# Optimization experiments

Measured on AMD Instinct MI355X. Metric: run time of the kernel, lower is better.

## Reference

```python
import jax, jax.numpy as jnp
import numpy as np

WS = 8   # window_size
SS = 4   # shift_size
NH = 8   # num_heads


def _shift_mask(ws, ss):
    """Faithful port of _create_shift_mask (returns [1,1,ws,ws])."""
    m = np.zeros((ws, ws), np.float32)
    cnt = 0
    for hs in (slice(0, ws - ss), slice(ws - ss, ws)):
        for wsl in (slice(0, ws - ss), slice(ws - ss, ws)):
            m[hs, wsl] = cnt
            cnt += 1
    shifted = np.roll(m, (-ss, -ss), (0, 1))
    return (m != shifted).astype(np.float32)[None, None]

_MASK = jnp.asarray(_shift_mask(WS, SS))  # all-ones when ss == ws/2 (as in source)


def window_partition(x, ws):
    # [B,C,H,W] -> [B*nWin, C, ws, ws]
    B, C, H, W = x.shape
    x = x.reshape(B, C, H // ws, ws, W // ws, ws)
    x = x.transpose(0, 2, 4, 1, 3, 5)
    return x.reshape(-1, C, ws, ws)


def window_merge(x, H, W, ws):
    # [B*nWin, C, ws, ws] -> [B,C,H,W]
    C = x.shape[1]
    B = x.shape[0] // ((H // ws) * (W // ws))
    x = x.reshape(B, H // ws, W // ws, C, ws, ws)
    x = x.transpose(0, 3, 1, 4, 2, 5)
    return x.reshape(B, C, H, W)


def conv1x1(x, w):
    # 1x1 conv, no bias: weight [Cout, Cin]
    return jnp.einsum('oc,bchw->bohw', w, x)


def win_attention(q, k, v, temperature):
    # q,k,v: [Bw, C, ws, ws]; temperature: [nh,1,1]
    Bw, C, wh, ww = q.shape
    hd = C // NH
    N = wh * ww
    def heads(t):
        return t.reshape(Bw, NH, hd, N).transpose(0, 1, 3, 2)  # [Bw,nh,N,hd]
    q, k, v = heads(q), heads(k), heads(v)
    attn = jnp.einsum('bhnd,bhmd->bhnm', q, k) * temperature  # temp broadcasts per-head
    attn = jax.nn.softmax(attn, axis=-1)
    out = jnp.einsum('bhnm,bhmd->bhnd', attn, v)
    return out.transpose(0, 1, 3, 2).reshape(Bw, C, wh, ww)


def _branch(x_q, x_kv, temperature, Wq, Wk, Wv, Wo):
    xq_w = window_partition(x_q, WS)
    xkv_w = window_partition(x_kv, WS)
    q = conv1x1(xq_w, Wq)
    k = conv1x1(xkv_w, Wk)
    v = conv1x1(xkv_w, Wv)
    a = win_attention(q, k, v, temperature)
    return conv1x1(a, Wo)  # [B*nWin, C, ws, ws]


def setup_inputs() -> dict:
    key = jax.random.key(0)
    ks = jax.random.split(key, 6)
    B, C, H, W = 2, 256, 192, 192
    return {
        'x_q': jax.random.normal(ks[0], (B, C, H, W), jnp.float32),
        'x_kv': jax.random.normal(ks[1], (B, C, H, W), jnp.float32),
        'temperature': jnp.ones((NH, 1, 1), jnp.float32),
        'Wq': jax.random.normal(ks[2], (C, C), jnp.float32) * 0.02,
        'Wk': jax.random.normal(ks[3], (C, C), jnp.float32) * 0.02,
        'Wv': jax.random.normal(ks[4], (C, C), jnp.float32) * 0.02,
        'Wo': jax.random.normal(ks[5], (C, C), jnp.float32) * 0.02,
    }


def reference(x_q, x_kv, temperature, Wq, Wk, Wv, Wo):
    B, C, H, W = x_q.shape
    # unshifted branch
    out_win = _branch(x_q, x_kv, temperature, Wq, Wk, Wv, Wo)
    out = window_merge(out_win, H, W, WS)
    # shifted branch
    xq_s = jnp.roll(x_q, shift=(-SS, -SS), axis=(2, 3))
    xkv_s = jnp.roll(x_kv, shift=(-SS, -SS), axis=(2, 3))
    out_s = _branch(xq_s, xkv_s, temperature, Wq, Wk, Wv, Wo)
    out_s = out_s * (1.0 - _MASK)  # zero overlap regions (all-ones mask here)
    out_s = window_merge(out_s, H, W, WS)
    out_s = jnp.roll(out_s, shift=(SS, SS), axis=(2, 3))
    return out + out_s
```

## Files before the change

### kernel.cpp

```cpp
#include <hip/hip_runtime.h>
#include <hip/hip_bf16.h>


typedef short bf16x4 __attribute__((ext_vector_type(4)));
typedef short bf16x8 __attribute__((ext_vector_type(8)));
typedef float f32x4  __attribute__((ext_vector_type(4)));
typedef unsigned short ushort_t;

#define MFMA_K16(A_, B_, C_) __builtin_amdgcn_mfma_f32_16x16x16bf16_1k((A_), (B_), (C_), 0, 0, 0)
#define MFMA_K32(A_, B_, C_) __builtin_amdgcn_mfma_f32_16x16x32_bf16((A_), (B_), (C_), 0, 0, 0)

__device__ __forceinline__ short f2b(float f) {
  __hip_bfloat16 h = __float2bfloat16(f);
  return __builtin_bit_cast(short, h);
}
__device__ __forceinline__ bf16x4 cvt4(f32x4 v, float sc) {
  bf16x4 r;
  r[0] = f2b(v[0] * sc); r[1] = f2b(v[1] * sc);
  r[2] = f2b(v[2] * sc); r[3] = f2b(v[3] * sc);
  return r;
}
__device__ __forceinline__ int PI(int p) { return (p ^ (p >> 3)) & 7; }

template<bool B16>
__device__ __forceinline__ bf16x8 ldw8(const void* W, int row, int c0) {
  if constexpr (B16) {
    return *(const bf16x8*)((const ushort_t*)W + (row << 8) + c0);
  } else {
    const float* p = (const float*)W + (row << 8) + c0;
    const float4 x = *(const float4*)p, y = *(const float4*)(p + 4);
    bf16x8 f;
    f[0] = f2b(x.x); f[1] = f2b(x.y); f[2] = f2b(x.z); f[3] = f2b(x.w);
    f[4] = f2b(y.x); f[5] = f2b(y.y); f[6] = f2b(y.z); f[7] = f2b(y.w);
    return f;
  }
}
__device__ __forceinline__ bf16x8 ldw8b(const ushort_t* W, int row, int c0) {
  return *(const bf16x8*)(W + (row << 8) + c0);
}

constexpr size_t BUFE = 9437184;

__global__ void wconv(const float* __restrict__ a, const float* __restrict__ b,
                      const float* __restrict__ c, const float* __restrict__ d,
                      ushort_t* __restrict__ o) {
  const int gid = blockIdx.x * 256 + threadIdx.x;
  const int which = gid >> 14;
  const int idx = (gid & 16383) * 4;
  const float* src = which == 0 ? a : which == 1 ? b : which == 2 ? c : d;
  const float4 v = *(const float4*)(src + idx);
  bf16x4 w; w[0] = f2b(v.x); w[1] = f2b(v.y); w[2] = f2b(v.z); w[3] = f2b(v.w);
  *(bf16x4*)(o + which * 65536 + idx) = w;
}

__global__ __launch_bounds__(256, 4) void g0_xt(
    const float* __restrict__ xq, const float* __restrict__ xkv,
    ushort_t* __restrict__ xtq, ushort_t* __restrict__ xtkv, int bbase)
{
  __shared__ __align__(16) ushort_t tile[64 * 72];
  const int tid = threadIdx.x;
  const int id = (blockIdx.x & 7) * (gridDim.x >> 3) + (blockIdx.x >> 3);
  int r = id;
  const int pxt = r % 576; r /= 576;
  const int ct = r & 3; r >>= 2;
  const int which = r & 1;
  const int bl = r >> 1;
  const float* src = which ? xkv : xq;
  ushort_t* dst = which ? xtkv : xtq;
  const size_t gib = (size_t)(bbase + bl) * BUFE;

  {
    const int cr = tid >> 2, seg = tid & 3;
    const float* p = src + gib + (size_t)(ct * 64 + cr) * 36864 + pxt * 64 + seg * 16;
    const float4 f0 = *(const float4*)p,       f1 = *(const float4*)(p + 4);
    const float4 f2 = *(const float4*)(p + 8), f3 = *(const float4*)(p + 12);
    bf16x8 a, b;
    a[0]=f2b(f0.x); a[1]=f2b(f0.y); a[2]=f2b(f0.z); a[3]=f2b(f0.w);
    a[4]=f2b(f1.x); a[5]=f2b(f1.y); a[6]=f2b(f1.z); a[7]=f2b(f1.w);
    b[0]=f2b(f2.x); b[1]=f2b(f2.y); b[2]=f2b(f2.z); b[3]=f2b(f2.w);
    b[4]=f2b(f3.x); b[5]=f2b(f3.y); b[6]=f2b(f3.z); b[7]=f2b(f3.w);
    *(bf16x8*)(tile + cr * 72 + seg * 16) = a;
    *(bf16x8*)(tile + cr * 72 + seg * 16 + 8) = b;
  }
  __syncthreads();
  {
    const int opx = tid >> 2, oseg = tid & 3;
    bf16x8 a, b;
    #pragma unroll
    for (int j = 0; j < 8; ++j) a[j] = tile[(oseg * 16 + j) * 72 + opx];
    #pragma unroll
    for (int j = 0; j < 8; ++j) b[j] = tile[(oseg * 16 + 8 + j) * 72 + opx];
    ushort_t* q = dst + (size_t)bl * BUFE + (size_t)(pxt * 64 + opx) * 256 + ct * 64 + oseg * 16;
    *(bf16x8*)q = a;
    *(bf16x8*)(q + 8) = b;
  }
}

__global__ __launch_bounds__(256, 4) void g1_qkv(
    const ushort_t* __restrict__ xtq, const ushort_t* __restrict__ xtkv,
    const ushort_t* __restrict__ Wq, const ushort_t* __restrict__ Wk,
    const ushort_t* __restrict__ Wv,
    ushort_t* __restrict__ qbuf, ushort_t* __restrict__ kbuf,
    ushort_t* __restrict__ vimg)
{
  __shared__ __align__(16) char smem[24576];
  const int tid = threadIdx.x, lane = tid & 63, wv4 = tid >> 6;
  const int l15 = lane & 15, g = lane >> 4;

  const int wid = (blockIdx.x & 7) * (gridDim.x >> 3) + (blockIdx.x >> 3);
  const int ct = wid % 6;
  int r = wid / 6;
  const int whalf = r & 1; r >>= 1;
  const int h = r % 192;
  const int bl = r / 192;
  const int wstart = whalf * 96, ph = h & 7;
  const int winbase = bl * 576 + (h >> 3) * 24 + whalf * 12;
  const int pxrow = h * 192 + wstart;

  const int mode = ct >> 1;
  const ushort_t* xs = ((mode == 0) ? xtq : xtkv) + (size_t)bl * BUFE;
  const ushort_t* W  = (mode == 0) ? Wq : (mode == 1) ? Wk : Wv;
  const int cobase = (ct & 1) * 128 + wv4 * 32;

  f32x4 acc[6][2];
  #pragma unroll
  for (int nt = 0; nt < 6; ++nt) { acc[nt][0] = {0,0,0,0}; acc[nt][1] = {0,0,0,0}; }

  #pragma unroll
  for (int ki = 0; ki < 2; ++ki) {
    if (ki) __syncthreads();
    #pragma unroll
    for (int j = 0; j < 6; ++j) {
      const int u = j * 256 + tid;
      const int t = u >> 4, ch = u & 15;
      const bf16x8 v = *(const bf16x8*)(xs + (size_t)(pxrow + t) * 256 + ki * 128 + ch * 8);
      const int sl = ch ^ (t & 7);
      *(bf16x8*)(smem + (unsigned)(t * 256 + sl * 16)) = v;
    }
    __syncthreads();
    #pragma unroll
    for (int sk = 0; sk < 4; ++sk) {
      const int c0 = ki * 128 + sk * 32 + g * 8;
      const bf16x8 w0 = ldw8b(W, cobase + l15,      c0);
      const bf16x8 w1 = ldw8b(W, cobase + 16 + l15, c0);
      #pragma unroll
      for (int nt = 0; nt < 6; ++nt) {
        const int t = nt * 16 + l15;
        const int lch = sk * 4 + g;
        const bf16x8 af = *(const bf16x8*)(smem + (unsigned)(t * 256 + ((lch ^ (t & 7)) << 4)));
        if (mode < 2) {
          acc[nt][0] = MFMA_K32(w0, af, acc[nt][0]);
          acc[nt][1] = MFMA_K32(w1, af, acc[nt][1]);
        } else {
          acc[nt][0] = MFMA_K32(af, w0, acc[nt][0]);
          acc[nt][1] = MFMA_K32(af, w1, acc[nt][1]);
        }
      }
    }
  }

  if (mode < 2) {
    ushort_t* dst = (mode == 0) ? qbuf : kbuf;
    #pragma unroll
    for (int nt = 0; nt < 6; ++nt)
      #pragma unroll
      for (int cj = 0; cj < 2; ++cj) {
        const int t = nt * 16 + l15;
        const int win = winbase + (t >> 3);
        const int pos = ph * 8 + (t & 7);
        const int co = cobase + cj * 16 + 4 * g;
        *(bf16x4*)(dst + (size_t)win * 16384 + pos * 256 + co) = cvt4(acc[nt][cj], 1.f);
      }
  } else {
    #pragma unroll
    for (int nt = 0; nt < 6; ++nt)
      #pragma unroll
      for (int dj = 0; dj < 2; ++dj) {
        const int t0 = nt * 16 + 4 * g;
        const int d = cobase + dj * 16 + l15;
        *(bf16x4*)(vimg + (size_t)bl * BUFE + (size_t)d * 36864 + pxrow + t0)
            = cvt4(acc[nt][dj], 1.f);
      }
  }
}

__global__ __launch_bounds__(256, 4) void attn2(
    const float* __restrict__ temp,
    const ushort_t* __restrict__ qbuf, const ushort_t* __restrict__ kbuf,
    const ushort_t* __restrict__ vimg, ushort_t* __restrict__ abuf)
{
  const int tid = threadIdx.x, lane = tid & 63, wv4 = tid >> 6;
  const int l15 = lane & 15, g = lane >> 4;

  const int wid = (blockIdx.x & 7) * (gridDim.x >> 3) + (blockIdx.x >> 3);
  const int hg = wid & 1;
  const int winL = wid >> 1;
  const int bl = winL / 576, rw = winL % 576;
  const int wh = rw / 24, ww = rw % 24;
  const int h = hg * 4 + wv4;
  const float tm = temp[h];
  const size_t wb = (size_t)winL * 16384;
  const int hb = h * 32;
  const f32x4 fzero = {0.f, 0.f, 0.f, 0.f};

  bf16x8 qf[4], kf[4];
  #pragma unroll
  for (int i = 0; i < 4; ++i) {
    qf[i] = *(const bf16x8*)(qbuf + wb + (i * 16 + l15) * 256 + hb + g * 8);
    kf[i] = *(const bf16x8*)(kbuf + wb + (i * 16 + l15) * 256 + hb + g * 8);
  }
  f32x4 s[4][4];
  #pragma unroll
  for (int mt = 0; mt < 4; ++mt)
    #pragma unroll
    for (int nt = 0; nt < 4; ++nt)
      s[mt][nt] = MFMA_K32(kf[mt], qf[nt], fzero);

  bf16x4 Pb[4][4];
  #pragma unroll
  for (int nt = 0; nt < 4; ++nt) {
    float mx = -1e30f;
    #pragma unroll
    for (int mt = 0; mt < 4; ++mt)
      #pragma unroll
      for (int rr = 0; rr < 4; ++rr) {
        const float v = s[mt][nt][rr] * tm;
        s[mt][nt][rr] = v;
        mx = fmaxf(mx, v);
      }
    mx = fmaxf(mx, __shfl_xor(mx, 16));
    mx = fmaxf(mx, __shfl_xor(mx, 32));
    float sum = 0.f;
    #pragma unroll
    for (int mt = 0; mt < 4; ++mt)
      #pragma unroll
      for (int rr = 0; rr < 4; ++rr) {
        const float p = __expf(s[mt][nt][rr] - mx);
        s[mt][nt][rr] = p;
        sum += p;
      }
    sum += __shfl_xor(sum, 16);
    sum += __shfl_xor(sum, 32);
    const float ri = 1.f / sum;
    #pragma unroll
    for (int mt = 0; mt < 4; ++mt) Pb[mt][nt] = cvt4(s[mt][nt], ri);
  }

  f32x4 pcd[2][4];
  #pragma unroll
  for (int dj = 0; dj < 2; ++dj)
    #pragma unroll
    for (int nt = 0; nt < 4; ++nt) pcd[dj][nt] = fzero;
  #pragma unroll
  for (int mt = 0; mt < 4; ++mt)
    #pragma unroll
    for (int dj = 0; dj < 2; ++dj) {
      const int d = hb + dj * 16 + l15;
      const bf16x4 vf = *(const bf16x4*)(vimg + (size_t)bl * BUFE + (size_t)d * 36864
                        + (wh * 8 + 2 * mt + (g >> 1)) * 192 + ww * 8 + 4 * (g & 1));
      #pragma unroll
      for (int nt = 0; nt < 4; ++nt)
        pcd[dj][nt] = MFMA_K16(vf, Pb[mt][nt], pcd[dj][nt]);
    }

  #pragma unroll
  for (int dj = 0; dj < 2; ++dj)
    #pragma unroll
    for (int nt = 0; nt < 4; ++nt) {
      const int pos = nt * 16 + l15;
      const int c0 = hb + dj * 16 + 4 * g;
      *(bf16x4*)(abuf + wb + pos * 256 + c0) = cvt4(pcd[dj][nt], 1.f);
    }
}

__global__ __launch_bounds__(256, 4) void k2_out(
    const ushort_t* __restrict__ Wo, const ushort_t* __restrict__ abuf,
    float* __restrict__ out, int bbase)
{
  __shared__ __align__(16) char smem[24576];
  const int tid = threadIdx.x, lane = tid & 63, wv4 = tid >> 6;
  const int l15 = lane & 15, g = lane >> 4;

  const int wid = (blockIdx.x & 7) * (gridDim.x >> 3) + (blockIdx.x >> 3);
  const int ct = wid & 1;
  int r = wid >> 1;
  const int whalf = r & 1; r >>= 1;
  const int h = r % 192, bl = r / 192;
  const int wh = h >> 3, ph = h & 7, wstart = whalf * 96;
  const int winbase = bl * 576 + wh * 24 + (wstart >> 3);

  f32x4 acc[6][2];
  #pragma unroll
  for (int nt = 0; nt < 6; ++nt) { acc[nt][0] = {0,0,0,0}; acc[nt][1] = {0,0,0,0}; }

  const int corow0 = ct * 128 + wv4 * 32 + l15;

  #pragma unroll
  for (int ki = 0; ki < 2; ++ki) {
    const int kb = ki * 128;
    if (ki) __syncthreads();
    #pragma unroll
    for (int j = 0; j < 6; ++j) {
      const int u = j * 256 + tid;
      const int t = u >> 4, ch = u & 15;
      const int win = winbase + (t >> 3);
      const int wpos = ph * 8 + (t & 7);
      const bf16x8 v = *(const bf16x8*)(abuf + (size_t)win * 16384 + wpos * 256 + kb + ch * 8);
      const int sl = ch ^ (t & 7);
      *(bf16x8*)(smem + (unsigned)(t * 256 + sl * 16)) = v;
    }
    __syncthreads();
    #pragma unroll
    for (int sk = 0; sk < 4; ++sk) {
      const int c0 = kb + sk * 32 + g * 8;
      const bf16x8 w0 = ldw8b(Wo, corow0,      c0);
      const bf16x8 w1 = ldw8b(Wo, corow0 + 16, c0);
      #pragma unroll
      for (int nt = 0; nt < 6; ++nt) {
        const int t = nt * 16 + l15;
        const int lch = sk * 4 + g;
        const bf16x8 af = *(const bf16x8*)(smem + (unsigned)(t * 256 + ((lch ^ (t & 7)) << 4)));
        acc[nt][0] = MFMA_K32(w0, af, acc[nt][0]);
        acc[nt][1] = MFMA_K32(w1, af, acc[nt][1]);
      }
    }
  }

  #pragma unroll
  for (int nt = 0; nt < 6; ++nt)
    #pragma unroll
    for (int cj = 0; cj < 2; ++cj) {
      const int t = nt * 16 + l15;
      #pragma unroll
      for (int rr = 0; rr < 4; ++rr) {
        const int co = ct * 128 + wv4 * 32 + cj * 16 + 4 * g + rr;
        out[(size_t)(bbase + bl) * BUFE + (size_t)co * 36864 + h * 192 + wstart + t]
            = acc[nt][cj][rr];
      }
    }
}

constexpr int SMEM_OLD = 65536;

template<int NT>
__device__ __forceinline__ void stage_half(char* dst, const float* __restrict__ src,
                                           int coff, int tid, size_t ibase, int xoff) {
  #pragma unroll
  for (int j = 0; j < 1024 / NT; ++j) {
    const int u = j * NT + tid;
    const int c = u >> 3, hr = u & 7;
    const size_t gg = ibase + (size_t)(c + coff) * 36864 + (size_t)(xoff + hr * 192);
    const float4 a0 = *(const float4*)(src + gg);
    const float4 a1 = *(const float4*)(src + gg + 4);
    const float vv[8] = {a0.x, a0.y, a0.z, a0.w, a1.x, a1.y, a1.z, a1.w};
    #pragma unroll
    for (int w = 0; w < 8; ++w) {
      const int pos = hr * 8 + w;
      const unsigned ad = (unsigned)(pos * 256 + (((c >> 3) ^ PI(pos)) << 4) + (c & 7) * 2);
      *(short*)(dst + ad) = f2b(vv[w]);
    }
  }
}
__device__ __forceinline__ bf16x8 xfrag8(const char* base, int kt, int nt, int l15, int g) {
  const int pos = nt * 16 + l15;
  const int c0 = kt * 32 + g * 8;
  const unsigned ad = (unsigned)(pos * 256 + (((c0 >> 3) ^ PI(pos)) << 4));
  return *(const bf16x8*)(base + ad);
}

template<bool WB16>
__global__ __launch_bounds__(512, 4) void wsmdta_old(
    const float* __restrict__ xq, const float* __restrict__ xkv,
    const float* __restrict__ temp,
    const void* __restrict__ Wq, const void* __restrict__ Wk,
    const void* __restrict__ Wv, const void* __restrict__ Wo,
    float* __restrict__ out)
{
  extern __shared__ __align__(16) char smem[];
  const int tid = threadIdx.x, lane = tid & 63, wv = tid >> 6;
  const int l15 = lane & 15, g = lane >> 4;
  const int bid = blockIdx.x;
  const int wid = (bid & 7) * 144 + (bid >> 3);
  const int b  = wid / 576, rw = wid - b * 576;
  const int wh = rw / 24,   ww = rw - wh * 24;
  const int xoff = wh * 1536 + ww * 8;
  const size_t ibase = (size_t)b * BUFE;
  const unsigned VB = 32768u + (unsigned)wv * 4096u;
  const f32x4 fzero = {0.f, 0.f, 0.f, 0.f};
  const int h = wv;
  const float tm = temp[h];

  f32x4 qcd[2][4];
  #pragma unroll
  for (int dj = 0; dj < 2; ++dj)
    #pragma unroll
    for (int nt = 0; nt < 4; ++nt) qcd[dj][nt] = fzero;
  #pragma unroll
  for (int half = 0; half < 2; ++half) {
    if (half) __syncthreads();
    stage_half<512>(smem, xq, half * 128, tid, ibase, xoff);
    __syncthreads();
    const int cg = half * 128;
    #pragma unroll
    for (int kt = 0; kt < 4; ++kt) {
      const bf16x8 w0 = ldw8<WB16>(Wq, h * 32 + l15,      cg + kt * 32 + g * 8);
      const bf16x8 w1 = ldw8<WB16>(Wq, h * 32 + 16 + l15, cg + kt * 32 + g * 8);
      #pragma unroll
      for (int nt = 0; nt < 4; ++nt) {
        const bf16x8 xf = xfrag8(smem, kt, nt, l15, g);
        qcd[0][nt] = MFMA_K32(w0, xf, qcd[0][nt]);
        qcd[1][nt] = MFMA_K32(w1, xf, qcd[1][nt]);
      }
    }
    __syncthreads();
  }
  bf16x4 qb[2][4];
  #pragma unroll
  for (int dj = 0; dj < 2; ++dj)
    #pragma unroll
    for (int nt = 0; nt < 4; ++nt) qb[dj][nt] = cvt4(qcd[dj][nt], 1.f);

  f32x4 kcd[2][4], vcd[2][4];
  #pragma unroll
  for (int dj = 0; dj < 2; ++dj)
    #pragma unroll
    for (int nt = 0; nt < 4; ++nt) { kcd[dj][nt] = fzero; vcd[dj][nt] = fzero; }
  #pragma unroll
  for (int half = 0; half < 2; ++half) {
    stage_half<512>(smem, xkv, half * 128, tid, ibase, xoff);
    __syncthreads();
    const int cg = half * 128;
    #pragma unroll
    for (int kt = 0; kt < 4; ++kt) {
      const bf16x8 wk0 = ldw8<WB16>(Wk, h * 32 + l15,      cg + kt * 32 + g * 8);
      const bf16x8 wk1 = ldw8<WB16>(Wk, h * 32 + 16 + l15, cg + kt * 32 + g * 8);
      const bf16x8 wv0 = ldw8<WB16>(Wv, h * 32 + l15,      cg + kt * 32 + g * 8);
      const bf16x8 wv1 = ldw8<WB16>(Wv, h * 32 + 16 + l15, cg + kt * 32 + g * 8);
      #pragma unroll
      for (int np = 0; np < 2; ++np) {
        const bf16x8 xf0 = xfrag8(smem, kt, np * 2,     l15, g);
        const bf16x8 xf1 = xfrag8(smem, kt, np * 2 + 1, l15, g);
        kcd[0][np*2]   = MFMA_K32(wk0, xf0, kcd[0][np*2]);
        kcd[1][np*2]   = MFMA_K32(wk1, xf0, kcd[1][np*2]);
        vcd[0][np*2]   = MFMA_K32(wv0, xf0, vcd[0][np*2]);
        vcd[1][np*2]   = MFMA_K32(wv1, xf0, vcd[1][np*2]);
        kcd[0][np*2+1] = MFMA_K32(wk0, xf1, kcd[0][np*2+1]);
        kcd[1][np*2+1] = MFMA_K32(wk1, xf1, kcd[1][np*2+1]);
        vcd[0][np*2+1] = MFMA_K32(wv0, xf1, vcd[0][np*2+1]);
        vcd[1][np*2+1] = MFMA_K32(wv1, xf1, vcd[1][np*2+1]);
      }
    }
    if (half == 0) __syncthreads();
  }
  bf16x4 kb[2][4];
  #pragma unroll
  for (int dj = 0; dj < 2; ++dj)
    #pragma unroll
    for (int mt = 0; mt < 4; ++mt) kb[dj][mt] = cvt4(kcd[dj][mt], 1.f);
  #pragma unroll
  for (int dj = 0; dj < 2; ++dj)
    #pragma unroll
    for (int mt = 0; mt < 4; ++mt) {
      const bf16x4 q = cvt4(vcd[dj][mt], 1.f);
      const int m = mt * 16 + l15;
      #pragma unroll
      for (int rr = 0; rr < 4; ++rr) {
        const int d = dj * 16 + 4 * g + rr;
        const unsigned ad = VB + (unsigned)(d * 128 + (((m >> 3) ^ (d & 7)) << 4) + (m & 7) * 2);
        *(short*)(smem + ad) = q[rr];
      }
    }
  f32x4 s[4][4];
  #pragma unroll
  for (int mt = 0; mt < 4; ++mt)
    #pragma unroll
    for (int nt = 0; nt < 4; ++nt) {
      s[mt][nt] = MFMA_K16(kb[0][mt], qb[0][nt], fzero);
      s[mt][nt] = MFMA_K16(kb[1][mt], qb[1][nt], s[mt][nt]);
    }
  bf16x4 Pb[4][4];
  #pragma unroll
  for (int nt = 0; nt < 4; ++nt) {
    float mx = -1e30f;
    #pragma unroll
    for (int mt = 0; mt < 4; ++mt)
      #pragma unroll
      for (int rr = 0; rr < 4; ++rr) {
        const float v = s[mt][nt][rr] * tm;
        s[mt][nt][rr] = v;
        mx = fmaxf(mx, v);
      }
    mx = fmaxf(mx, __shfl_xor(mx, 16));
    mx = fmaxf(mx, __shfl_xor(mx, 32));
    float sum = 0.f;
    #pragma unroll
    for (int mt = 0; mt < 4; ++mt)
      #pragma unroll
      for (int rr = 0; rr < 4; ++rr) {
        const float p = __expf(s[mt][nt][rr] - mx);
        s[mt][nt][rr] = p;
        sum += p;
      }
    sum += __shfl_xor(sum, 16);
    sum += __shfl_xor(sum, 32);
    const float ri = 1.f / sum;
    #pragma unroll
    for (int mt = 0; mt < 4; ++mt) Pb[mt][nt] = cvt4(s[mt][nt], ri);
  }
  f32x4 pcd[2][4];
  #pragma unroll
  for (int dj = 0; dj < 2; ++dj)
    #pragma unroll
    for (int nt = 0; nt < 4; ++nt) pcd[dj][nt] = fzero;
  #pragma unroll
  for (int mt = 0; mt < 4; ++mt)
    #pragma unroll
    for (int dj = 0; dj < 2; ++dj) {
      const int d = dj * 16 + l15;
      const unsigned ad = VB + (unsigned)(d * 128 + (((mt * 2 + (g >> 1)) ^ (d & 7)) << 4) + (g & 1) * 8);
      const bf16x4 vf = *(const bf16x4*)(smem + ad);
      #pragma unroll
      for (int nt = 0; nt < 4; ++nt)
        pcd[dj][nt] = MFMA_K16(vf, Pb[mt][nt], pcd[dj][nt]);
    }
  __syncthreads();
  #pragma unroll
  for (int dj = 0; dj < 2; ++dj)
    #pragma unroll
    for (int nt = 0; nt < 4; ++nt) {
      const bf16x4 q = cvt4(pcd[dj][nt], 1.f);
      const int pos = nt * 16 + l15;
      const int c0 = h * 32 + dj * 16 + 4 * g;
      const unsigned ad = (unsigned)(pos * 512 + (((c0 >> 3) ^ PI(pos)) << 4) + (c0 & 7) * 2);
      *(bf16x4*)(smem + ad) = q;
    }
  __syncthreads();
  f32x4 ocd[4][2];
  #pragma unroll
  for (int nt = 0; nt < 4; ++nt) { ocd[nt][0] = fzero; ocd[nt][1] = fzero; }
  {
    bf16x8 w0 = ldw8<WB16>(Wo, wv * 32 + l15,      g * 8);
    bf16x8 w1 = ldw8<WB16>(Wo, wv * 32 + 16 + l15, g * 8);
    #pragma unroll
    for (int ks = 0; ks < 8; ++ks) {
      bf16x8 n0, n1;
      if (ks < 7) {
        n0 = ldw8<WB16>(Wo, wv * 32 + l15,      (ks + 1) * 32 + g * 8);
        n1 = ldw8<WB16>(Wo, wv * 32 + 16 + l15, (ks + 1) * 32 + g * 8);
      }
      #pragma unroll
      for (int nt = 0; nt < 4; ++nt) {
        const int pos = nt * 16 + l15;
        const unsigned ad = (unsigned)(pos * 512 + (((ks * 4 + g) ^ PI(pos)) << 4));
        const bf16x8 af = *(const bf16x8*)(smem + ad);
        ocd[nt][0] = MFMA_K32(af, w0, ocd[nt][0]);
        ocd[nt][1] = MFMA_K32(af, w1, ocd[nt][1]);
      }
      if (ks < 7) { w0 = n0; w1 = n1; }
    }
  }
  #pragma unroll
  for (int nt = 0; nt < 4; ++nt)
    #pragma unroll
    for (int ctj = 0; ctj < 2; ++ctj) {
      const int c_out = wv * 32 + ctj * 16 + l15;
      const int h_out = nt * 2 + (g >> 1);
      const int w0o = 4 * (g & 1);
      float4 v;
      v.x = ocd[nt][ctj][0]; v.y = ocd[nt][ctj][1];
      v.z = ocd[nt][ctj][2]; v.w = ocd[nt][ctj][3];
      *(float4*)(out + ibase + (size_t)c_out * 36864 + (size_t)(xoff + h_out * 192 + w0o)) = v;
    }
}

extern "C" void kernel_launch(void* const* d_in, const int* in_sizes, int n_in,
                              void* d_out, int out_size, void* d_ws, size_t ws_size,
                              hipStream_t stream) {
  (void)in_sizes; (void)n_in; (void)out_size;
  const float* xq   = (const float*)d_in[0];
  const float* xkv  = (const float*)d_in[1];
  const float* temp = (const float*)d_in[2];
  const float* Wq   = (const float*)d_in[3];
  const float* Wk   = (const float*)d_in[4];
  const float* Wv   = (const float*)d_in[5];
  const float* Wo   = (const float*)d_in[6];
  float* out = (float*)d_out;

  const size_t W_ELEMS = 262144;
  auto need = [&](int nb) {
    return (W_ELEMS + 5u * (size_t)nb * BUFE) * sizeof(ushort_t);
  };
  ushort_t* wsb = (ushort_t*)d_ws;

  auto run = [&](int bbase, int nb) {
    ushort_t* base = wsb + W_ELEMS;
    ushort_t* xtq  = base;
    ushort_t* xtkv = xtq  + (size_t)nb * BUFE;
    ushort_t* qb   = xtkv + (size_t)nb * BUFE;
    ushort_t* kb   = qb   + (size_t)nb * BUFE;
    ushort_t* vb   = kb   + (size_t)nb * BUFE;
    g0_xt<<<dim3(nb * 4608), dim3(256), 0, stream>>>(xq, xkv, xtq, xtkv, bbase);
    g1_qkv<<<dim3(nb * 2304), dim3(256), 0, stream>>>(
        xtq, xtkv, wsb, wsb + 65536, wsb + 131072, qb, kb, vb);
    attn2<<<dim3(nb * 1152), dim3(256), 0, stream>>>(temp, qb, kb, vb, qb);
    k2_out<<<dim3(nb * 768), dim3(256), 0, stream>>>(wsb + 196608, qb, out, bbase);
  };

  if (ws_size >= need(2)) {
    wconv<<<dim3(256), dim3(256), 0, stream>>>(Wq, Wk, Wv, Wo, wsb);
    run(0, 2);
  } else if (ws_size >= need(1)) {
    wconv<<<dim3(256), dim3(256), 0, stream>>>(Wq, Wk, Wv, Wo, wsb);
    run(0, 1);
    run(1, 1);
  } else if (ws_size >= W_ELEMS * sizeof(ushort_t)) {
    wconv<<<dim3(256), dim3(256), 0, stream>>>(Wq, Wk, Wv, Wo, wsb);
    (void)hipFuncSetAttribute((const void*)&wsmdta_old<true>,
                              hipFuncAttributeMaxDynamicSharedMemorySize, SMEM_OLD);
    wsmdta_old<true><<<dim3(1152), dim3(512), SMEM_OLD, stream>>>(
        xq, xkv, temp, wsb, wsb + 65536, wsb + 131072, wsb + 196608, out);
  } else {
    (void)hipFuncSetAttribute((const void*)&wsmdta_old<false>,
                              hipFuncAttributeMaxDynamicSharedMemorySize, SMEM_OLD);
    wsmdta_old<false><<<dim3(1152), dim3(512), SMEM_OLD, stream>>>(
        xq, xkv, temp, Wq, Wk, Wv, Wo, out);
  }
}
```

Before: 190.5 us.

## Stage QKV epilogue through LDS for 16-byte coalesced stores; hoist weight loads

The QKV projection kernel now writes its bf16 accumulators into shared memory and reads them back as contiguous 16-byte chunks. Each output row is then stored to global memory as full coalesced vectors instead of scattered 8-byte writes. Weight fragments for each K-half are loaded into registers before the activation tile is staged, so global weight loads can overlap the LDS fill. In exchange the kernel uses more shared memory and extra barriers, and holding the weight fragments raises register pressure, which could reduce occupancy.

New measurement: 184.5 us, median of 3. 1.03x faster.

```diff
diff --git a/kernel.cpp b/kernel.cpp
--- a/kernel.cpp
+++ b/kernel.cpp
@@ -103,7 +103,7 @@
     ushort_t* __restrict__ qbuf, ushort_t* __restrict__ kbuf,
     ushort_t* __restrict__ vimg)
 {
-  __shared__ __align__(16) char smem[24576];
+  __shared__ __align__(16) char smem[26624];
   const int tid = threadIdx.x, lane = tid & 63, wv4 = tid >> 6;
   const int l15 = lane & 15, g = lane >> 4;
 
@@ -113,14 +113,15 @@
   const int whalf = r & 1; r >>= 1;
   const int h = r % 192;
   const int bl = r / 192;
-  const int wstart = whalf * 96, ph = h & 7;
+  const int ph = h & 7;
   const int winbase = bl * 576 + (h >> 3) * 24 + whalf * 12;
-  const int pxrow = h * 192 + wstart;
+  const int pxrow = h * 192 + whalf * 96;
 
   const int mode = ct >> 1;
   const ushort_t* xs = ((mode == 0) ? xtq : xtkv) + (size_t)bl * BUFE;
   const ushort_t* W  = (mode == 0) ? Wq : (mode == 1) ? Wk : Wv;
-  const int cobase = (ct & 1) * 128 + wv4 * 32;
+  const int chalf = (ct & 1) * 128;
+  const int cobase = chalf + wv4 * 32;
 
   f32x4 acc[6][2];
   #pragma unroll
@@ -128,6 +129,13 @@
 
   #pragma unroll
   for (int ki = 0; ki < 2; ++ki) {
+    bf16x8 wf[4][2];
+    #pragma unroll
+    for (int sk = 0; sk < 4; ++sk) {
+      const int c0 = ki * 128 + sk * 32 + g * 8;
+      wf[sk][0] = ldw8b(W, cobase + l15,      c0);
+      wf[sk][1] = ldw8b(W, cobase + 16 + l15, c0);
+    }
     if (ki) __syncthreads();
     #pragma unroll
     for (int j = 0; j < 6; ++j) {
@@ -140,47 +148,59 @@
     __syncthreads();
     #pragma unroll
     for (int sk = 0; sk < 4; ++sk) {
-      const int c0 = ki * 128 + sk * 32 + g * 8;
-      const bf16x8 w0 = ldw8b(W, cobase + l15,      c0);
-      const bf16x8 w1 = ldw8b(W, cobase + 16 + l15, c0);
       #pragma unroll
       for (int nt = 0; nt < 6; ++nt) {
         const int t = nt * 16 + l15;
         const int lch = sk * 4 + g;
         const bf16x8 af = *(const bf16x8*)(smem + (unsigned)(t * 256 + ((lch ^ (t & 7)) << 4)));
         if (mode < 2) {
-          acc[nt][0] = MFMA_K32(w0, af, acc[nt][0]);
-          acc[nt][1] = MFMA_K32(w1, af, acc[nt][1]);
+          acc[nt][0] = MFMA_K32(wf[sk][0], af, acc[nt][0]);
+          acc[nt][1] = MFMA_K32(wf[sk][1], af, acc[nt][1]);
         } else {
-          acc[nt][0] = MFMA_K32(af, w0, acc[nt][0]);
-          acc[nt][1] = MFMA_K32(af, w1, acc[nt][1]);
+          acc[nt][0] = MFMA_K32(af, wf[sk][0], acc[nt][0]);
+          acc[nt][1] = MFMA_K32(af, wf[sk][1], acc[nt][1]);
         }
       }
     }
   }
+  __syncthreads();
 
   if (mode < 2) {
-    ushort_t* dst = (mode == 0) ? qbuf : kbuf;
     #pragma unroll
     for (int nt = 0; nt < 6; ++nt)
       #pragma unroll
       for (int cj = 0; cj < 2; ++cj) {
         const int t = nt * 16 + l15;
-        const int win = winbase + (t >> 3);
-        const int pos = ph * 8 + (t & 7);
-        const int co = cobase + cj * 16 + 4 * g;
-        *(bf16x4*)(dst + (size_t)win * 16384 + pos * 256 + co) = cvt4(acc[nt][cj], 1.f);
-      }
+        const int bb = (wv4 * 4 + cj * 2 + (g >> 1)) ^ (t & 7);
+        *(bf16x4*)(smem + (unsigned)(t * 256 + bb * 16 + (g & 1) * 8)) = cvt4(acc[nt][cj], 1.f);
+      }
+    __syncthreads();
+    ushort_t* dst = (mode == 0) ? qbuf : kbuf;
+    #pragma unroll
+    for (int j = 0; j < 6; ++j) {
+      const int u = j * 256 + tid;
+      const int t = u >> 4, ch = u & 15;
+      const bf16x8 v = *(const bf16x8*)(smem + (unsigned)(t * 256 + ((ch ^ (t & 7)) << 4)));
+      const int win = winbase + (t >> 3);
+      const int pos = ph * 8 + (t & 7);
+      *(bf16x8*)(dst + (size_t)win * 16384 + pos * 256 + chalf + ch * 8) = v;
+    }
   } else {
     #pragma unroll
     for (int nt = 0; nt < 6; ++nt)
       #pragma unroll
       for (int dj = 0; dj < 2; ++dj) {
-        const int t0 = nt * 16 + 4 * g;
-        const int d = cobase + dj * 16 + l15;
-        *(bf16x4*)(vimg + (size_t)bl * BUFE + (size_t)d * 36864 + pxrow + t0)
-            = cvt4(acc[nt][dj], 1.f);
-      }
+        const int dl = wv4 * 32 + dj * 16 + l15;
+        *(bf16x4*)(smem + (unsigned)(dl * 208 + (nt * 16 + 4 * g) * 2)) = cvt4(acc[nt][dj], 1.f);
+      }
+    __syncthreads();
+    #pragma unroll
+    for (int j = 0; j < 6; ++j) {
+      const int u = j * 256 + tid;
+      const int dl = u / 12, ch = u - dl * 12;
+      const bf16x8 v = *(const bf16x8*)(smem + (unsigned)(dl * 208 + ch * 16));
+      *(bf16x8*)(vimg + (size_t)bl * BUFE + (size_t)(chalf + dl) * 36864 + pxrow + ch * 8) = v;
+    }
   }
 }
 
```
